# Optimization experiments

Hardware: AMD Instinct MI355X
Metric: run time of the kernel (lower is better)

The kernel has to match this reference:

```python
import jax, jax.numpy as jnp
import numpy as np

X_DIM = 512
C_DIM = 512
T = 32768
I_DIM = X_DIM + C_DIM


def setup_inputs() -> dict:
    key = jax.random.key(0)
    ks = jax.random.split(key, 9)
    s = 1.0 / np.sqrt(I_DIM)  # torch nn.Linear default init range
    def lin(kw, kb):
        w = jax.random.uniform(kw, (C_DIM, I_DIM), jnp.float32, -s, s)
        b = jax.random.uniform(kb, (C_DIM,), jnp.float32, -s, s)
        return w, b
    wf_w, wf_b = lin(ks[0], ks[1])
    wi_w, wi_b = lin(ks[2], ks[3])
    wc_w, wc_b = lin(ks[4], ks[5])
    wo_w, wo_b = lin(ks[6], ks[7])
    x_list = jax.random.normal(ks[8], (T, X_DIM), jnp.float32)
    return {"x_list": x_list, "wf_w": wf_w, "wf_b": wf_b, "wi_w": wi_w,
            "wi_b": wi_b, "wc_w": wc_w, "wc_b": wc_b, "wo_w": wo_w, "wo_b": wo_b}


def reference(x_list, wf_w, wf_b, wi_w, wi_b, wc_w, wc_b, wo_w, wo_b):
    c_dim = wf_w.shape[0]
    # Fuse the four gate projections into one GEMV per step (same math:
    # torch Linear y = i @ W.T + b, applied per gate then concatenated).
    W = jnp.concatenate([wf_w, wi_w, wc_w, wo_w], axis=0)  # [4*c_dim, i_dim]
    b = jnp.concatenate([wf_b, wi_b, wc_b, wo_b], axis=0)  # [4*c_dim]

    def step(carry, x):
        c, h = carry
        i = jnp.concatenate([x, h])          # [i_dim]
        g = W @ i + b                         # [4*c_dim]
        ff = jax.nn.sigmoid(g[:c_dim])
        ii = jax.nn.sigmoid(g[c_dim:2 * c_dim])
        cc = jnp.tanh(g[2 * c_dim:3 * c_dim])
        oo = jax.nn.sigmoid(g[3 * c_dim:])
        c = ff * c + ii * cc
        h = jnp.tanh(c) * oo
        return (c, h), None

    init = (jnp.zeros((c_dim,), x_list.dtype), jnp.zeros((c_dim,), x_list.dtype))
    (c, h), _ = jax.lax.scan(step, init, x_list)
    return (c, h)
```

## Files before the change

### kernel.cpp

```cpp
#include <hip/hip_runtime.h>
#include <hip/hip_bf16.h>
#include <cstdint>


#define T_TOTAL 32768
#define NBLK 64

__device__ __forceinline__ float sigm(float x) {
    return 1.0f / (1.0f + __expf(-x));
}
__device__ __forceinline__ float tanh_fast(float x) {
    float ax = fabsf(x);
    float e = __expf(2.0f * ax);
    float t = 1.0f - 2.0f / (e + 1.0f);
    return copysignf(t, x);
}

__global__ __launch_bounds__(256, 1) void lstm_gemm_x(
    const float* __restrict__ x,
    const float* __restrict__ wf, const float* __restrict__ wi,
    const float* __restrict__ wc, const float* __restrict__ wo,
    const float* __restrict__ bf, const float* __restrict__ bi,
    const float* __restrict__ bc, const float* __restrict__ bo,
    float* __restrict__ gx, int t0, int tend)
{
    __shared__ float xs[16][512];
    const int tid = threadIdx.x;
    const int tt0 = t0 + blockIdx.x * 16;
    const int j0  = blockIdx.y * 128;

    #pragma unroll
    for (int i = 0; i < 8; ++i) {
        int idx  = tid + i * 256;
        int trow = idx >> 7, kq = idx & 127;
        int t    = tt0 + trow;
        float4 v = make_float4(0.f, 0.f, 0.f, 0.f);
        if (t < tend) v = *(const float4*)(x + (size_t)t * 512 + kq * 4);
        *(float4*)&xs[trow][kq * 4] = v;
    }
    __syncthreads();

    const int j  = j0 + (tid & 127);
    const int th = tid >> 7;
    const int g  = j >> 9;
    const int jg = j & 511;
    const float* Wg = (g == 0) ? wf : (g == 1) ? wi : (g == 2) ? wc : wo;
    const float* Bg = (g == 0) ? bf : (g == 1) ? bi : (g == 2) ? bc : bo;
    const float* wrow = Wg + (size_t)jg * 1024;

    float acc[8];
    #pragma unroll
    for (int i = 0; i < 8; ++i) acc[i] = 0.f;

    for (int k = 0; k < 512; k += 4) {
        float4 w4 = *(const float4*)(wrow + k);
        #pragma unroll
        for (int tt = 0; tt < 8; ++tt) {
            float4 x4 = *(const float4*)&xs[th * 8 + tt][k];
            acc[tt] = fmaf(w4.x, x4.x, acc[tt]);
            acc[tt] = fmaf(w4.y, x4.y, acc[tt]);
            acc[tt] = fmaf(w4.z, x4.z, acc[tt]);
            acc[tt] = fmaf(w4.w, x4.w, acc[tt]);
        }
    }

    const float bias = Bg[jg];
    const int   obase = (jg >> 3) * 32 + (jg & 7) * 4 + g;
    #pragma unroll
    for (int tt = 0; tt < 8; ++tt) {
        int t = tt0 + th * 8 + tt;
        if (t < tend) gx[(size_t)(t - t0) * 2048 + obase] = acc[tt] + bias;
    }
}

__global__ __launch_bounds__(256, 1) void lstm_serial(
    const float* __restrict__ wf, const float* __restrict__ wi,
    const float* __restrict__ wc, const float* __restrict__ wo,
    const float* __restrict__ gx,
    unsigned long long* __restrict__ hdq,
    float* __restrict__ cstate,
    int t0, int steps, float* __restrict__ out)
{
    __shared__ alignas(16) float4 wlds4[4096];
    __shared__ alignas(16) float  hl[2][512];
    const int b   = blockIdx.x;
    const int tid = threadIdx.x;
    const int r   = tid >> 5;
    const int seg = tid & 31;
    const int w   = tid >> 6;
    const int l   = tid & 63;

    #pragma unroll
    for (int k = 0; k < 16; ++k) {
        int idx = k * 256 + tid;
        int ll  = idx & 63;
        int jj  = (idx >> 6) & 3;
        int gg  = (idx >> 8) & 3;
        int ww  = idx >> 10;
        const float* Wp = (gg == 0) ? wf : (gg == 1) ? wi : (gg == 2) ? wc : wo;
        int row = b * 8 + ww * 2 + (ll >> 5);
        wlds4[idx] = *(const float4*)(Wp + (size_t)row * 1024 + 512
                                      + 4 * (ll & 31) + 128 * jj);
    }
    float cold = cstate[b * 8 + r];
    __syncthreads();

    const float4* hl4  = (const float4*)hl;
    const int     wbase = w * 1024 + l;

    for (int s = 0; s < steps; ++s) {
        const int t  = t0 + s;
        const int sp = (t & 1) ^ 1;
        const int sc = t & 1;

        float4 gx4 = make_float4(0.f, 0.f, 0.f, 0.f);
        if (seg == 0)
            gx4 = *(const float4*)(gx + (size_t)s * 2048 + b * 32 + r * 4);

        float4 w00 = wlds4[wbase +   0], w01 = wlds4[wbase +  64];
        float4 w02 = wlds4[wbase + 128], w03 = wlds4[wbase + 192];
        float4 w10 = wlds4[wbase + 256], w11 = wlds4[wbase + 320];
        float4 w12 = wlds4[wbase + 384], w13 = wlds4[wbase + 448];
        float4 w20 = wlds4[wbase + 512], w21 = wlds4[wbase + 576];
        float4 w22 = wlds4[wbase + 640], w23 = wlds4[wbase + 704];
        float4 w30 = wlds4[wbase + 768], w31 = wlds4[wbase + 832];
        float4 w32 = wlds4[wbase + 896], w33 = wlds4[wbase + 960];

        if (tid < 64) {
            const unsigned need = (unsigned)t;
            const unsigned long long* src = hdq + (size_t)sp * 512 + tid;
            unsigned long long v0, v1, v2, v3, v4, v5, v6, v7;
            int guard = 0;
            bool ok = false;
            do {
                v0 = __hip_atomic_load(src,       __ATOMIC_RELAXED, __HIP_MEMORY_SCOPE_AGENT);
                v1 = __hip_atomic_load(src + 64,  __ATOMIC_RELAXED, __HIP_MEMORY_SCOPE_AGENT);
                v2 = __hip_atomic_load(src + 128, __ATOMIC_RELAXED, __HIP_MEMORY_SCOPE_AGENT);
                v3 = __hip_atomic_load(src + 192, __ATOMIC_RELAXED, __HIP_MEMORY_SCOPE_AGENT);
                v4 = __hip_atomic_load(src + 256, __ATOMIC_RELAXED, __HIP_MEMORY_SCOPE_AGENT);
                v5 = __hip_atomic_load(src + 320, __ATOMIC_RELAXED, __HIP_MEMORY_SCOPE_AGENT);
                v6 = __hip_atomic_load(src + 384, __ATOMIC_RELAXED, __HIP_MEMORY_SCOPE_AGENT);
                v7 = __hip_atomic_load(src + 448, __ATOMIC_RELAXED, __HIP_MEMORY_SCOPE_AGENT);
                ok = ((unsigned)(v0 >> 32) == need) & ((unsigned)(v1 >> 32) == need)
                   & ((unsigned)(v2 >> 32) == need) & ((unsigned)(v3 >> 32) == need)
                   & ((unsigned)(v4 >> 32) == need) & ((unsigned)(v5 >> 32) == need)
                   & ((unsigned)(v6 >> 32) == need) & ((unsigned)(v7 >> 32) == need);
            } while (!ok && ++guard < (1 << 20));
            hl[sp][tid]       = __uint_as_float((unsigned)v0);
            hl[sp][tid + 64]  = __uint_as_float((unsigned)v1);
            hl[sp][tid + 128] = __uint_as_float((unsigned)v2);
            hl[sp][tid + 192] = __uint_as_float((unsigned)v3);
            hl[sp][tid + 256] = __uint_as_float((unsigned)v4);
            hl[sp][tid + 320] = __uint_as_float((unsigned)v5);
            hl[sp][tid + 384] = __uint_as_float((unsigned)v6);
            hl[sp][tid + 448] = __uint_as_float((unsigned)v7);
        }
        __syncthreads();

        float4 h0 = hl4[sp * 128 + seg];
        float4 h1 = hl4[sp * 128 + seg + 32];
        float4 h2 = hl4[sp * 128 + seg + 64];
        float4 h3 = hl4[sp * 128 + seg + 96];

        float a0 = 0.f, a1 = 0.f, a2 = 0.f, a3 = 0.f;
        a0 = fmaf(w00.x, h0.x, a0); a0 = fmaf(w00.y, h0.y, a0);
        a0 = fmaf(w00.z, h0.z, a0); a0 = fmaf(w00.w, h0.w, a0);
        a0 = fmaf(w01.x, h1.x, a0); a0 = fmaf(w01.y, h1.y, a0);
        a0 = fmaf(w01.z, h1.z, a0); a0 = fmaf(w01.w, h1.w, a0);
        a0 = fmaf(w02.x, h2.x, a0); a0 = fmaf(w02.y, h2.y, a0);
        a0 = fmaf(w02.z, h2.z, a0); a0 = fmaf(w02.w, h2.w, a0);
        a0 = fmaf(w03.x, h3.x, a0); a0 = fmaf(w03.y, h3.y, a0);
        a0 = fmaf(w03.z, h3.z, a0); a0 = fmaf(w03.w, h3.w, a0);

        a1 = fmaf(w10.x, h0.x, a1); a1 = fmaf(w10.y, h0.y, a1);
        a1 = fmaf(w10.z, h0.z, a1); a1 = fmaf(w10.w, h0.w, a1);
        a1 = fmaf(w11.x, h1.x, a1); a1 = fmaf(w11.y, h1.y, a1);
        a1 = fmaf(w11.z, h1.z, a1); a1 = fmaf(w11.w, h1.w, a1);
        a1 = fmaf(w12.x, h2.x, a1); a1 = fmaf(w12.y, h2.y, a1);
        a1 = fmaf(w12.z, h2.z, a1); a1 = fmaf(w12.w, h2.w, a1);
        a1 = fmaf(w13.x, h3.x, a1); a1 = fmaf(w13.y, h3.y, a1);
        a1 = fmaf(w13.z, h3.z, a1); a1 = fmaf(w13.w, h3.w, a1);

        a2 = fmaf(w20.x, h0.x, a2); a2 = fmaf(w20.y, h0.y, a2);
        a2 = fmaf(w20.z, h0.z, a2); a2 = fmaf(w20.w, h0.w, a2);
        a2 = fmaf(w21.x, h1.x, a2); a2 = fmaf(w21.y, h1.y, a2);
        a2 = fmaf(w21.z, h1.z, a2); a2 = fmaf(w21.w, h1.w, a2);
        a2 = fmaf(w22.x, h2.x, a2); a2 = fmaf(w22.y, h2.y, a2);
        a2 = fmaf(w22.z, h2.z, a2); a2 = fmaf(w22.w, h2.w, a2);
        a2 = fmaf(w23.x, h3.x, a2); a2 = fmaf(w23.y, h3.y, a2);
        a2 = fmaf(w23.z, h3.z, a2); a2 = fmaf(w23.w, h3.w, a2);

        a3 = fmaf(w30.x, h0.x, a3); a3 = fmaf(w30.y, h0.y, a3);
        a3 = fmaf(w30.z, h0.z, a3); a3 = fmaf(w30.w, h0.w, a3);
        a3 = fmaf(w31.x, h1.x, a3); a3 = fmaf(w31.y, h1.y, a3);
        a3 = fmaf(w31.z, h1.z, a3); a3 = fmaf(w31.w, h1.w, a3);
        a3 = fmaf(w32.x, h2.x, a3); a3 = fmaf(w32.y, h2.y, a3);
        a3 = fmaf(w32.z, h2.z, a3); a3 = fmaf(w32.w, h2.w, a3);
        a3 = fmaf(w33.x, h3.x, a3); a3 = fmaf(w33.y, h3.y, a3);
        a3 = fmaf(w33.z, h3.z, a3); a3 = fmaf(w33.w, h3.w, a3);

        #pragma unroll
        for (int m = 1; m < 32; m <<= 1) {
            a0 += __shfl_xor(a0, m);
            a1 += __shfl_xor(a1, m);
            a2 += __shfl_xor(a2, m);
            a3 += __shfl_xor(a3, m);
        }

        if (seg == 0) {
            float ff  = sigm(a0 + gx4.x);
            float iiv = sigm(a1 + gx4.y);
            float ccv = tanh_fast(a2 + gx4.z);
            float ov  = sigm(a3 + gx4.w);
            cold = fmaf(ff, cold, iiv * ccv);
            float hnew = tanh_fast(cold) * ov;
            unsigned long long tv = ((unsigned long long)(unsigned)(t + 1) << 32)
                                  | (unsigned long long)__float_as_uint(hnew);
            atomicExch(hdq + (size_t)sc * 512 + b * 8 + r, tv);
            if (t == T_TOTAL - 1) {
                out[b * 8 + r]       = cold;
                out[512 + b * 8 + r] = hnew;
            }
        }
    }

    if (seg == 0) cstate[b * 8 + r] = cold;
}

extern "C" void kernel_launch(void* const* d_in, const int* in_sizes, int n_in,
                              void* d_out, int out_size, void* d_ws, size_t ws_size,
                              hipStream_t stream)
{
    const float* x  = (const float*)d_in[0];
    const float* wf = (const float*)d_in[1];
    const float* bf = (const float*)d_in[2];
    const float* wi = (const float*)d_in[3];
    const float* bi = (const float*)d_in[4];
    const float* wc = (const float*)d_in[5];
    const float* bc = (const float*)d_in[6];
    const float* wo = (const float*)d_in[7];
    const float* bo = (const float*)d_in[8];
    float* out = (float*)d_out;

    char* wsb = (char*)d_ws;
    unsigned long long* hdq = (unsigned long long*)wsb;
    float* cst = (float*)(wsb + 8192);
    const size_t metaBytes = 8192 + 2048;
    float* gxbuf = (float*)(wsb + metaBytes);

    size_t gxCapSteps = (ws_size > metaBytes)
                        ? (ws_size - metaBytes) / (2048 * sizeof(float)) : 0;
    int CH = (gxCapSteps < (size_t)T_TOTAL) ? (int)gxCapSteps : T_TOTAL;
    CH &= ~15;
    if (CH < 16) CH = 16;

    hipMemsetAsync(wsb, 0, metaBytes, stream);

    for (int t0 = 0; t0 < T_TOTAL; t0 += CH) {
        int tend  = t0 + CH; if (tend > T_TOTAL) tend = T_TOTAL;
        int steps = tend - t0;
        dim3 ggrid((steps + 15) / 16, 16);
        lstm_gemm_x<<<ggrid, 256, 0, stream>>>(x, wf, wi, wc, wo,
                                               bf, bi, bc, bo, gxbuf, t0, tend);
        lstm_serial<<<NBLK, 256, 0, stream>>>(wf, wi, wc, wo, gxbuf,
                                              hdq, cst, t0, steps, out);
    }
}
```

Measured before the change: 68.56 ms.

## Add a dedicated polling wavefront that prefetches next-step hidden state during compute

The serial LSTM kernel grows from 256 to 320 threads. Wave 0 becomes a dedicated poller: while the other four waves compute the current step's gate GEMV and state update, it spins on the global h exchange buffer for the next step. It now re-loads only the entries still pending instead of all eight each round. Each step keeps a single barrier, and the aim is to overlap cross-block synchronisation latency with compute. The cost is an extra wavefront per block, and the critical path still includes the cross-block handoff.

```diff
diff --git a/kernel.cpp b/kernel.cpp
--- a/kernel.cpp
+++ b/kernel.cpp
@@ -73,7 +73,7 @@
     }
 }
 
-__global__ __launch_bounds__(256, 1) void lstm_serial(
+__global__ __launch_bounds__(320, 1) void lstm_serial(
     const float* __restrict__ wf, const float* __restrict__ wi,
     const float* __restrict__ wc, const float* __restrict__ wo,
     const float* __restrict__ gx,
@@ -83,148 +83,173 @@
 {
     __shared__ alignas(16) float4 wlds4[4096];
     __shared__ alignas(16) float  hl[2][512];
-    const int b   = blockIdx.x;
-    const int tid = threadIdx.x;
-    const int r   = tid >> 5;
-    const int seg = tid & 31;
-    const int w   = tid >> 6;
-    const int l   = tid & 63;
-
-    #pragma unroll
-    for (int k = 0; k < 16; ++k) {
-        int idx = k * 256 + tid;
-        int ll  = idx & 63;
-        int jj  = (idx >> 6) & 3;
-        int gg  = (idx >> 8) & 3;
-        int ww  = idx >> 10;
-        const float* Wp = (gg == 0) ? wf : (gg == 1) ? wi : (gg == 2) ? wc : wo;
-        int row = b * 8 + ww * 2 + (ll >> 5);
-        wlds4[idx] = *(const float4*)(Wp + (size_t)row * 1024 + 512
-                                      + 4 * (ll & 31) + 128 * jj);
-    }
-    float cold = cstate[b * 8 + r];
+
+    const int b    = blockIdx.x;
+    const int tid  = threadIdx.x;
+    const int wave = tid >> 6;
+    const int lane = tid & 63;
+
+    float cold = 0.f;
+    if (wave >= 1) {
+        const int ct = tid - 64;
+        #pragma unroll
+        for (int k = 0; k < 16; ++k) {
+            int idx = k * 256 + ct;
+            int ll  = idx & 63;
+            int jj  = (idx >> 6) & 3;
+            int gg  = (idx >> 8) & 3;
+            int ww  = idx >> 10;
+            const float* Wp = (gg == 0) ? wf : (gg == 1) ? wi
+                             : (gg == 2) ? wc : wo;
+            int row = b * 8 + ww * 2 + (ll >> 5);
+            wlds4[idx] = *(const float4*)(Wp + (size_t)row * 1024 + 512
+                                          + 4 * (ll & 31) + 128 * jj);
+        }
+        cold = cstate[b * 8 + (ct >> 5)];
+    }
+
+    if (wave == 0) {
+        const int sp0 = (t0 & 1) ^ 1;
+        const unsigned need = (unsigned)t0;
+        const unsigned long long* src = hdq + (size_t)sp0 * 512 + lane;
+        unsigned pend = 0xFFu;
+        int guard = 0;
+        while (pend && ++guard < (1 << 20)) {
+            #pragma unroll
+            for (int i = 0; i < 8; ++i) {
+                if (pend & (1u << i)) {
+                    unsigned long long v = __hip_atomic_load(src + i * 64,
+                        __ATOMIC_RELAXED, __HIP_MEMORY_SCOPE_AGENT);
+                    if ((unsigned)(v >> 32) == need) {
+                        hl[sp0][lane + i * 64] = __uint_as_float((unsigned)v);
+                        pend &= ~(1u << i);
+                    }
+                }
+            }
+        }
+    }
     __syncthreads();
 
-    const float4* hl4  = (const float4*)hl;
-    const int     wbase = w * 1024 + l;
+    const float4* hl4 = (const float4*)hl;
 
     for (int s = 0; s < steps; ++s) {
         const int t  = t0 + s;
         const int sp = (t & 1) ^ 1;
         const int sc = t & 1;
 
-        float4 gx4 = make_float4(0.f, 0.f, 0.f, 0.f);
-        if (seg == 0)
-            gx4 = *(const float4*)(gx + (size_t)s * 2048 + b * 32 + r * 4);
-
-        float4 w00 = wlds4[wbase +   0], w01 = wlds4[wbase +  64];
-        float4 w02 = wlds4[wbase + 128], w03 = wlds4[wbase + 192];
-        float4 w10 = wlds4[wbase + 256], w11 = wlds4[wbase + 320];
-        float4 w12 = wlds4[wbase + 384], w13 = wlds4[wbase + 448];
-        float4 w20 = wlds4[wbase + 512], w21 = wlds4[wbase + 576];
-        float4 w22 = wlds4[wbase + 640], w23 = wlds4[wbase + 704];
-        float4 w30 = wlds4[wbase + 768], w31 = wlds4[wbase + 832];
-        float4 w32 = wlds4[wbase + 896], w33 = wlds4[wbase + 960];
-
-        if (tid < 64) {
-            const unsigned need = (unsigned)t;
-            const unsigned long long* src = hdq + (size_t)sp * 512 + tid;
-            unsigned long long v0, v1, v2, v3, v4, v5, v6, v7;
-            int guard = 0;
-            bool ok = false;
-            do {
-                v0 = __hip_atomic_load(src,       __ATOMIC_RELAXED, __HIP_MEMORY_SCOPE_AGENT);
-                v1 = __hip_atomic_load(src + 64,  __ATOMIC_RELAXED, __HIP_MEMORY_SCOPE_AGENT);
-                v2 = __hip_atomic_load(src + 128, __ATOMIC_RELAXED, __HIP_MEMORY_SCOPE_AGENT);
-                v3 = __hip_atomic_load(src + 192, __ATOMIC_RELAXED, __HIP_MEMORY_SCOPE_AGENT);
-                v4 = __hip_atomic_load(src + 256, __ATOMIC_RELAXED, __HIP_MEMORY_SCOPE_AGENT);
-                v5 = __hip_atomic_load(src + 320, __ATOMIC_RELAXED, __HIP_MEMORY_SCOPE_AGENT);
-                v6 = __hip_atomic_load(src + 384, __ATOMIC_RELAXED, __HIP_MEMORY_SCOPE_AGENT);
-                v7 = __hip_atomic_load(src + 448, __ATOMIC_RELAXED, __HIP_MEMORY_SCOPE_AGENT);
-                ok = ((unsigned)(v0 >> 32) == need) & ((unsigned)(v1 >> 32) == need)
-                   & ((unsigned)(v2 >> 32) == need) & ((unsigned)(v3 >> 32) == need)
-                   & ((unsigned)(v4 >> 32) == need) & ((unsigned)(v5 >> 32) == need)
-                   & ((unsigned)(v6 >> 32) == need) & ((unsigned)(v7 >> 32) == need);
-            } while (!ok && ++guard < (1 << 20));
-            hl[sp][tid]       = __uint_as_float((unsigned)v0);
-            hl[sp][tid + 64]  = __uint_as_float((unsigned)v1);
-            hl[sp][tid + 128] = __uint_as_float((unsigned)v2);
-            hl[sp][tid + 192] = __uint_as_float((unsigned)v3);
-            hl[sp][tid + 256] = __uint_as_float((unsigned)v4);
-            hl[sp][tid + 320] = __uint_as_float((unsigned)v5);
-            hl[sp][tid + 384] = __uint_as_float((unsigned)v6);
-            hl[sp][tid + 448] = __uint_as_float((unsigned)v7);
+        if (wave == 0) {
+            if (s < steps - 1) {
+                const unsigned need = (unsigned)(t + 1);
+                const unsigned long long* src = hdq + (size_t)sc * 512 + lane;
+                unsigned pend = 0xFFu;
+                int guard = 0;
+                while (pend && ++guard < (1 << 20)) {
+                    #pragma unroll
+                    for (int i = 0; i < 8; ++i) {
+                        if (pend & (1u << i)) {
+                            unsigned long long v = __hip_atomic_load(src + i * 64,
+                                __ATOMIC_RELAXED, __HIP_MEMORY_SCOPE_AGENT);
+                            if ((unsigned)(v >> 32) == need) {
+                                hl[sc][lane + i * 64] =
+                                    __uint_as_float((unsigned)v);
+                                pend &= ~(1u << i);
+                            }
+                        }
+                    }
+                }
+            }
+        } else {
+            const int ct  = tid - 64;
+            const int r   = ct >> 5;
+            const int seg = ct & 31;
+            const int w   = ct >> 6;
+            const int l   = ct & 63;
+            const int wb  = w * 1024 + l;
+
+            float4 gx4 = make_float4(0.f, 0.f, 0.f, 0.f);
+            if (seg == 0)
+                gx4 = *(const float4*)(gx + (size_t)s * 2048 + b * 32 + r * 4);
+
+            float4 w00 = wlds4[wb +   0], w01 = wlds4[wb +  64];
+            float4 w02 = wlds4[wb + 128], w03 = wlds4[wb + 192];
+            float4 w10 = wlds4[wb + 256], w11 = wlds4[wb + 320];
+            float4 w12 = wlds4[wb + 384], w13 = wlds4[wb + 448];
+            float4 w20 = wlds4[wb + 512], w21 = wlds4[wb + 576];
+            float4 w22 = wlds4[wb + 640], w23 = wlds4[wb + 704];
+            float4 w30 = wlds4[wb + 768], w31 = wlds4[wb + 832];
+            float4 w32 = wlds4[wb + 896], w33 = wlds4[wb + 960];
+
+            float4 h0 = hl4[sp * 128 + seg];
+            float4 h1 = hl4[sp * 128 + seg + 32];
+            float4 h2 = hl4[sp * 128 + seg + 64];
+            float4 h3 = hl4[sp * 128 + seg + 96];
+
+            float a0 = 0.f, a1 = 0.f, a2 = 0.f, a3 = 0.f;
+            a0 = fmaf(w00.x, h0.x, a0); a0 = fmaf(w00.y, h0.y, a0);
+            a0 = fmaf(w00.z, h0.z, a0); a0 = fmaf(w00.w, h0.w, a0);
+            a0 = fmaf(w01.x, h1.x, a0); a0 = fmaf(w01.y, h1.y, a0);
+            a0 = fmaf(w01.z, h1.z, a0); a0 = fmaf(w01.w, h1.w, a0);
+            a0 = fmaf(w02.x, h2.x, a0); a0 = fmaf(w02.y, h2.y, a0);
+            a0 = fmaf(w02.z, h2.z, a0); a0 = fmaf(w02.w, h2.w, a0);
+            a0 = fmaf(w03.x, h3.x, a0); a0 = fmaf(w03.y, h3.y, a0);
+            a0 = fmaf(w03.z, h3.z, a0); a0 = fmaf(w03.w, h3.w, a0);
+
+            a1 = fmaf(w10.x, h0.x, a1); a1 = fmaf(w10.y, h0.y, a1);
+            a1 = fmaf(w10.z, h0.z, a1); a1 = fmaf(w10.w, h0.w, a1);
+            a1 = fmaf(w11.x, h1.x, a1); a1 = fmaf(w11.y, h1.y, a1);
+            a1 = fmaf(w11.z, h1.z, a1); a1 = fmaf(w11.w, h1.w, a1);
+            a1 = fmaf(w12.x, h2.x, a1); a1 = fmaf(w12.y, h2.y, a1);
+            a1 = fmaf(w12.z, h2.z, a1); a1 = fmaf(w12.w, h2.w, a1);
+            a1 = fmaf(w13.x, h3.x, a1); a1 = fmaf(w13.y, h3.y, a1);
+            a1 = fmaf(w13.z, h3.z, a1); a1 = fmaf(w13.w, h3.w, a1);
+
+            a2 = fmaf(w20.x, h0.x, a2); a2 = fmaf(w20.y, h0.y, a2);
+            a2 = fmaf(w20.z, h0.z, a2); a2 = fmaf(w20.w, h0.w, a2);
+            a2 = fmaf(w21.x, h1.x, a2); a2 = fmaf(w21.y, h1.y, a2);
+            a2 = fmaf(w21.z, h1.z, a2); a2 = fmaf(w21.w, h1.w, a2);
+            a2 = fmaf(w22.x, h2.x, a2); a2 = fmaf(w22.y, h2.y, a2);
+            a2 = fmaf(w22.z, h2.z, a2); a2 = fmaf(w22.w, h2.w, a2);
+            a2 = fmaf(w23.x, h3.x, a2); a2 = fmaf(w23.y, h3.y, a2);
+            a2 = fmaf(w23.z, h3.z, a2); a2 = fmaf(w23.w, h3.w, a2);
+
+            a3 = fmaf(w30.x, h0.x, a3); a3 = fmaf(w30.y, h0.y, a3);
+            a3 = fmaf(w30.z, h0.z, a3); a3 = fmaf(w30.w, h0.w, a3);
+            a3 = fmaf(w31.x, h1.x, a3); a3 = fmaf(w31.y, h1.y, a3);
+            a3 = fmaf(w31.z, h1.z, a3); a3 = fmaf(w31.w, h1.w, a3);
+            a3 = fmaf(w32.x, h2.x, a3); a3 = fmaf(w32.y, h2.y, a3);
+            a3 = fmaf(w32.z, h2.z, a3); a3 = fmaf(w32.w, h2.w, a3);
+            a3 = fmaf(w33.x, h3.x, a3); a3 = fmaf(w33.y, h3.y, a3);
+            a3 = fmaf(w33.z, h3.z, a3); a3 = fmaf(w33.w, h3.w, a3);
+
+            #pragma unroll
+            for (int m = 1; m < 32; m <<= 1) {
+                a0 += __shfl_xor(a0, m);
+                a1 += __shfl_xor(a1, m);
+                a2 += __shfl_xor(a2, m);
+                a3 += __shfl_xor(a3, m);
+            }
+
+            if (seg == 0) {
+                float ff  = sigm(a0 + gx4.x);
+                float iiv = sigm(a1 + gx4.y);
+                float ccv = tanh_fast(a2 + gx4.z);
+                float ov  = sigm(a3 + gx4.w);
+                cold = fmaf(ff, cold, iiv * ccv);
+                float hnew = tanh_fast(cold) * ov;
+                unsigned long long tv =
+                    ((unsigned long long)(unsigned)(t + 1) << 32)
+                    | (unsigned long long)__float_as_uint(hnew);
+                atomicExch(hdq + (size_t)sc * 512 + b * 8 + r, tv);
+                if (t == T_TOTAL - 1) {
+                    out[b * 8 + r]       = cold;
+                    out[512 + b * 8 + r] = hnew;
+                }
+            }
         }
         __syncthreads();
-
-        float4 h0 = hl4[sp * 128 + seg];
-        float4 h1 = hl4[sp * 128 + seg + 32];
-        float4 h2 = hl4[sp * 128 + seg + 64];
-        float4 h3 = hl4[sp * 128 + seg + 96];
-
-        float a0 = 0.f, a1 = 0.f, a2 = 0.f, a3 = 0.f;
-        a0 = fmaf(w00.x, h0.x, a0); a0 = fmaf(w00.y, h0.y, a0);
-        a0 = fmaf(w00.z, h0.z, a0); a0 = fmaf(w00.w, h0.w, a0);
-        a0 = fmaf(w01.x, h1.x, a0); a0 = fmaf(w01.y, h1.y, a0);
-        a0 = fmaf(w01.z, h1.z, a0); a0 = fmaf(w01.w, h1.w, a0);
-        a0 = fmaf(w02.x, h2.x, a0); a0 = fmaf(w02.y, h2.y, a0);
-        a0 = fmaf(w02.z, h2.z, a0); a0 = fmaf(w02.w, h2.w, a0);
-        a0 = fmaf(w03.x, h3.x, a0); a0 = fmaf(w03.y, h3.y, a0);
-        a0 = fmaf(w03.z, h3.z, a0); a0 = fmaf(w03.w, h3.w, a0);
-
-        a1 = fmaf(w10.x, h0.x, a1); a1 = fmaf(w10.y, h0.y, a1);
-        a1 = fmaf(w10.z, h0.z, a1); a1 = fmaf(w10.w, h0.w, a1);
-        a1 = fmaf(w11.x, h1.x, a1); a1 = fmaf(w11.y, h1.y, a1);
-        a1 = fmaf(w11.z, h1.z, a1); a1 = fmaf(w11.w, h1.w, a1);
-        a1 = fmaf(w12.x, h2.x, a1); a1 = fmaf(w12.y, h2.y, a1);
-        a1 = fmaf(w12.z, h2.z, a1); a1 = fmaf(w12.w, h2.w, a1);
-        a1 = fmaf(w13.x, h3.x, a1); a1 = fmaf(w13.y, h3.y, a1);
-        a1 = fmaf(w13.z, h3.z, a1); a1 = fmaf(w13.w, h3.w, a1);
-
-        a2 = fmaf(w20.x, h0.x, a2); a2 = fmaf(w20.y, h0.y, a2);
-        a2 = fmaf(w20.z, h0.z, a2); a2 = fmaf(w20.w, h0.w, a2);
-        a2 = fmaf(w21.x, h1.x, a2); a2 = fmaf(w21.y, h1.y, a2);
-        a2 = fmaf(w21.z, h1.z, a2); a2 = fmaf(w21.w, h1.w, a2);
-        a2 = fmaf(w22.x, h2.x, a2); a2 = fmaf(w22.y, h2.y, a2);
-        a2 = fmaf(w22.z, h2.z, a2); a2 = fmaf(w22.w, h2.w, a2);
-        a2 = fmaf(w23.x, h3.x, a2); a2 = fmaf(w23.y, h3.y, a2);
-        a2 = fmaf(w23.z, h3.z, a2); a2 = fmaf(w23.w, h3.w, a2);
-
-        a3 = fmaf(w30.x, h0.x, a3); a3 = fmaf(w30.y, h0.y, a3);
-        a3 = fmaf(w30.z, h0.z, a3); a3 = fmaf(w30.w, h0.w, a3);
-        a3 = fmaf(w31.x, h1.x, a3); a3 = fmaf(w31.y, h1.y, a3);
-        a3 = fmaf(w31.z, h1.z, a3); a3 = fmaf(w31.w, h1.w, a3);
-        a3 = fmaf(w32.x, h2.x, a3); a3 = fmaf(w32.y, h2.y, a3);
-        a3 = fmaf(w32.z, h2.z, a3); a3 = fmaf(w32.w, h2.w, a3);
-        a3 = fmaf(w33.x, h3.x, a3); a3 = fmaf(w33.y, h3.y, a3);
-        a3 = fmaf(w33.z, h3.z, a3); a3 = fmaf(w33.w, h3.w, a3);
-
-        #pragma unroll
-        for (int m = 1; m < 32; m <<= 1) {
-            a0 += __shfl_xor(a0, m);
-            a1 += __shfl_xor(a1, m);
-            a2 += __shfl_xor(a2, m);
-            a3 += __shfl_xor(a3, m);
-        }
-
-        if (seg == 0) {
-            float ff  = sigm(a0 + gx4.x);
-            float iiv = sigm(a1 + gx4.y);
-            float ccv = tanh_fast(a2 + gx4.z);
-            float ov  = sigm(a3 + gx4.w);
-            cold = fmaf(ff, cold, iiv * ccv);
-            float hnew = tanh_fast(cold) * ov;
-            unsigned long long tv = ((unsigned long long)(unsigned)(t + 1) << 32)
-                                  | (unsigned long long)__float_as_uint(hnew);
-            atomicExch(hdq + (size_t)sc * 512 + b * 8 + r, tv);
-            if (t == T_TOTAL - 1) {
-                out[b * 8 + r]       = cold;
-                out[512 + b * 8 + r] = hnew;
-            }
-        }
-    }
-
-    if (seg == 0) cstate[b * 8 + r] = cold;
+    }
+
+    if (wave >= 1 && (tid & 31) == 0) cstate[b * 8 + ((tid - 64) >> 5)] = cold;
 }
 
 extern "C" void kernel_launch(void* const* d_in, const int* in_sizes, int n_in,
@@ -262,7 +287,7 @@
         dim3 ggrid((steps + 15) / 16, 16);
         lstm_gemm_x<<<ggrid, 256, 0, stream>>>(x, wf, wi, wc, wo,
                                                bf, bi, bc, bo, gxbuf, t0, tend);
-        lstm_serial<<<NBLK, 256, 0, stream>>>(wf, wi, wc, wo, gxbuf,
+        lstm_serial<<<NBLK, 320, 0, stream>>>(wf, wi, wc, wo, gxbuf,
                                               hdq, cst, t0, steps, out);
     }
 }
```

New measurement: 128.5 ms. +87.4%, slower.
